# Kernel tuning notes

Hardware: AMD Instinct MI355X
Metric: run time of the kernel (lower is better)

## Reference

```python
import jax, jax.numpy as jnp
import numpy as np

K = 3
N_SENSOR = 10   # num_sensor N (forced by reshape(-1,10,10))
ADJ_N = 5       # adjacency size (forced by reshape(-1,5,5))
T_LEN = 4096    # seq_len
BATCH = 1024    # batch_size == num_of_filters (forced by output accumulation)


def _scaled_laplacian(W):
    # L_tilde = 2L/lambda_max - I, L = D - W (W symmetric -> eigvalsh valid)
    D = jnp.diag(jnp.sum(W, axis=1))
    L = D - W
    lam_max = jnp.max(jnp.linalg.eigvalsh(L))
    return (2.0 * L) / lam_max - jnp.eye(W.shape[0], dtype=W.dtype)


def _cheb_polynomials(L_tilde, K):
    polys = [jnp.eye(L_tilde.shape[0], dtype=L_tilde.dtype), L_tilde]
    for _ in range(2, K):
        polys.append(2.0 * (L_tilde @ polys[-1]) - polys[-2])
    return jnp.stack(polys[:K])  # (K, 5, 5)


def setup_inputs() -> dict:
    key = jax.random.key(0)
    kx, ka, ks, kt = jax.random.split(key, 4)
    x = jax.random.normal(kx, (T_LEN, BATCH, N_SENSOR), dtype=jnp.float32)
    W = jax.random.uniform(ka, (ADJ_N, ADJ_N), dtype=jnp.float32)
    # symmetric, zero-diagonal adjacency so the Laplacian is symmetric PSD-ish
    adj_mx = (W + W.T) * 0.5 * (1.0 - jnp.eye(ADJ_N, dtype=jnp.float32))
    spatial_attention = jax.random.uniform(ks, (BATCH, N_SENSOR, N_SENSOR), dtype=jnp.float32)
    Theta = jax.random.normal(kt, (K, N_SENSOR, BATCH), dtype=jnp.float32)  # (K, num_of_timesteps=10, num_of_filters=B)
    return {"x": x, "adj_mx": adj_mx, "spatial_attention": spatial_attention, "Theta": Theta}


def reference(x, adj_mx, spatial_attention, Theta):
    # adj path is detached in the torch code (cpu().detach().numpy())
    L_tilde = _scaled_laplacian(jax.lax.stop_gradient(adj_mx))
    cheb = _cheb_polynomials(L_tilde, K)                 # (K, 5, 5)
    T, B, N = x.shape                                    # (T, B, 10)
    x_t = jnp.swapaxes(x, 0, 2)                          # (10, B, T)
    sa = spatial_attention.reshape(-1, ADJ_N, ADJ_N)     # (4B, 5, 5)
    output = jnp.zeros((T, B, N), dtype=x.dtype)
    for k in range(K):
        T_k_with_at = (cheb[k] * sa).reshape(-1, N, N)   # (B, 10, 10)
        lhs = jnp.swapaxes(T_k_with_at, 0, 2)            # (10, 10, B)
        rhs = jnp.matmul(lhs, x_t)                       # (10, 10, B) @ (10, B, T) -> (10, 10, T)
        out_k = jnp.matmul(jnp.swapaxes(rhs, 1, 2), Theta[k])  # (10, T, 10) @ (10, B) -> (10, T, B)
        output = output + jnp.transpose(out_k, (1, 2, 0))       # (T, B, 10)
    return jax.nn.relu(output[..., None])                # (T, B, 10, 1)
```

## Files before the change

kernel.cpp:

```cpp
#include <hip/hip_runtime.h>
#include <math.h>

#define TLEN 4096
#define NB   1024
#define NS   10
#define KC   64
#define NCHK 16
#define BUF_U32 10240

typedef __attribute__((ext_vector_type(8))) short s16x8;
typedef __attribute__((ext_vector_type(4))) float f32x4;
typedef __attribute__((ext_vector_type(2))) float f32x2;

static __device__ __forceinline__ unsigned cvtpk(float lo, float hi) {
  unsigned r;
  asm("v_cvt_pk_bf16_f32 %0, %1, %2" : "=v"(r) : "v"(lo), "v"(hi));
  return r;
}
static __device__ __forceinline__ int swz(int P, int L) {
  return P*64 + (L ^ ((P ^ (P >> 2)) & 7));
}
static __device__ __forceinline__ void lbar() {
  asm volatile("s_waitcnt lgkmcnt(0)" ::: "memory");
  __builtin_amdgcn_s_barrier();
}

__global__ __launch_bounds__(512) void fused_k(
    const float* __restrict__ x, const float* __restrict__ sa,
    const float* __restrict__ adj, const float* __restrict__ theta,
    float* __restrict__ out) {
  __shared__ __align__(16) unsigned buf[BUF_U32];
  __shared__ __align__(16) unsigned S2[16*52];
  __shared__ float ck[300];
  const int tid = threadIdx.x;
  const int l   = tid & 63;
  const int t0  = blockIdx.x * 16;

  const int w   = tid >> 6;
  const int bp  = tid / 10;
  const int rm  = tid - bp*10;
  const int q   = rm >> 1;
  const int th  = rm & 1;
  const int gq  = rm;
  const int ksx = bp >> 4;
  const int kgx = (bp & 15) >> 2;
  const int jwx = bp & 3;
  const int n0  = 2*w, n1 = 2*w + 1;

  f32x4 acc0 = {0.f,0.f,0.f,0.f}, acc1 = {0.f,0.f,0.f,0.f};
  f32x2 xlo[8], xhi[8], slo[5], shi[5];

  float pL[5][5], pv[5];
  if (tid == 320) {
    float Wm[5][5];
    #pragma unroll
    for (int r = 0; r < 5; ++r)
      #pragma unroll
      for (int c = 0; c < 5; ++c) Wm[r][c] = adj[r*5+c];
    #pragma unroll
    for (int r = 0; r < 5; ++r) {
      float d = 0.f;
      #pragma unroll
      for (int c = 0; c < 5; ++c) d += Wm[r][c];
      #pragma unroll
      for (int c = 0; c < 5; ++c) pL[r][c] = (r==c ? d : 0.f) - Wm[r][c];
    }
    pv[0]=0.7f; pv[1]=-1.1f; pv[2]=0.9f; pv[3]=-0.8f; pv[4]=1.3f;
  }

  if (tid < 320) {
    const float* xb = x + (size_t)(t0 + th*8)*(NB*NS) + (size_t)(2*bp)*NS + 2*q;
    #pragma unroll
    for (int r = 0; r < 8; ++r) {
      xlo[r] = __builtin_nontemporal_load((const f32x2*)(xb + r*(NB*NS)));
      xhi[r] = __builtin_nontemporal_load((const f32x2*)(xb + r*(NB*NS) + NS));
    }
    const float* sb = sa + (size_t)(2*bp)*100 + gq*10;
    #pragma unroll
    for (int e = 0; e < 5; ++e) {
      slo[e] = *(const f32x2*)(sb + 2*e);
      shi[e] = *(const f32x2*)(sb + 100 + 2*e);
    }
    #pragma unroll
    for (int r = 0; r < 8; ++r) {
      const int L = kgx*16 + th*8 + r;
      buf[swz((2*q  )*2 + ksx, L)*4 + jwx] = cvtpk(xlo[r].x, xhi[r].x);
      buf[swz((2*q+1)*2 + ksx, L)*4 + jwx] = cvtpk(xlo[r].y, xhi[r].y);
    }
    #pragma unroll
    for (int e = 0; e < 5; ++e) {
      const int L = kgx*16 + gq;
      buf[5120 + swz((2*e  )*2 + ksx, L)*4 + jwx] = cvtpk(slo[e].x, shi[e].x);
      buf[5120 + swz((2*e+1)*2 + ksx, L)*4 + jwx] = cvtpk(slo[e].y, shi[e].y);
    }
  }

  for (int c = 0; c < NCHK; ++c) {
    lbar();
    if (tid < 320) {
      if (c + 1 < NCHK) {
        const int bc = (c+1)*KC;
        const float* xb = x + (size_t)(t0 + th*8)*(NB*NS)
                            + (size_t)(bc + 2*bp)*NS + 2*q;
        #pragma unroll
        for (int r = 0; r < 8; ++r) {
          xlo[r] = __builtin_nontemporal_load((const f32x2*)(xb + r*(NB*NS)));
          xhi[r] = __builtin_nontemporal_load((const f32x2*)(xb + r*(NB*NS) + NS));
        }
        const float* sb = sa + (size_t)(bc + 2*bp)*100 + gq*10;
        #pragma unroll
        for (int e = 0; e < 5; ++e) {
          slo[e] = *(const f32x2*)(sb + 2*e);
          shi[e] = *(const f32x2*)(sb + 100 + 2*e);
        }
      }
      const s16x8* XBf = (const s16x8*)buf;
      const s16x8* ASf = (const s16x8*)(buf + 5120);
      #pragma unroll
      for (int ks = 0; ks < 2; ++ks) {
        acc0 = __builtin_amdgcn_mfma_f32_16x16x32_bf16(
                 ASf[swz(n0*2+ks, l)], XBf[swz(n0*2+ks, l)], acc0, 0, 0, 0);
        acc1 = __builtin_amdgcn_mfma_f32_16x16x32_bf16(
                 ASf[swz(n1*2+ks, l)], XBf[swz(n1*2+ks, l)], acc1, 0, 0, 0);
      }
    } else if (tid == 320 && c < 12) {
      #pragma unroll
      for (int it = 0; it < 8; ++it) {
        float wv[5];
        #pragma unroll
        for (int r = 0; r < 5; ++r) {
          float s = 0.f;
          #pragma unroll
          for (int cc = 0; cc < 5; ++cc) s += pL[r][cc]*pv[cc];
          wv[r] = s;
        }
        float s = fabsf(wv[0])+fabsf(wv[1])+fabsf(wv[2])+fabsf(wv[3])+fabsf(wv[4]);
        float inv = 1.f/s;
        #pragma unroll
        for (int r = 0; r < 5; ++r) pv[r] = wv[r]*inv;
      }
    }
    lbar();
    if (tid < 320 && c + 1 < NCHK) {
      #pragma unroll
      for (int r = 0; r < 8; ++r) {
        const int L = kgx*16 + th*8 + r;
        buf[swz((2*q  )*2 + ksx, L)*4 + jwx] = cvtpk(xlo[r].x, xhi[r].x);
        buf[swz((2*q+1)*2 + ksx, L)*4 + jwx] = cvtpk(xlo[r].y, xhi[r].y);
      }
      #pragma unroll
      for (int e = 0; e < 5; ++e) {
        const int L = kgx*16 + gq;
        buf[5120 + swz((2*e  )*2 + ksx, L)*4 + jwx] = cvtpk(slo[e].x, shi[e].x);
        buf[5120 + swz((2*e+1)*2 + ksx, L)*4 + jwx] = cvtpk(slo[e].y, shi[e].y);
      }
    }
  }

  if (tid == 320) {
    float num = 0.f, den = 0.f;
    #pragma unroll
    for (int r = 0; r < 5; ++r) {
      float s = 0.f;
      #pragma unroll
      for (int cc = 0; cc < 5; ++cc) s += pL[r][cc]*pv[cc];
      num += pv[r]*s; den += pv[r]*pv[r];
    }
    const float lam = num/den;
    float Lt[5][5], T2[5][5];
    #pragma unroll
    for (int r = 0; r < 5; ++r)
      #pragma unroll
      for (int cc = 0; cc < 5; ++cc)
        Lt[r][cc] = 2.f*pL[r][cc]/lam - (r==cc ? 1.f : 0.f);
    #pragma unroll
    for (int r = 0; r < 5; ++r)
      #pragma unroll
      for (int cc = 0; cc < 5; ++cc) {
        float s = 0.f;
        #pragma unroll
        for (int j = 0; j < 5; ++j) s += Lt[r][j]*Lt[j][cc];
        T2[r][cc] = 2.f*s - (r==cc ? 1.f : 0.f);
      }
    #pragma unroll
    for (int p = 0; p < 10; ++p)
      #pragma unroll
      for (int nn = 0; nn < 10; ++nn) {
        const int m = (10*p+nn) % 25, r = m/5, cc = m%5;
        ck[0*100 + p*10+nn] = (r==cc ? 1.f : 0.f);
        ck[1*100 + p*10+nn] = Lt[r][cc];
        ck[2*100 + p*10+nn] = T2[r][cc];
      }
  }
  if (tid < 320) {
    const int pg = (l >> 4) * 4;
    const int tl = l & 15;
    unsigned* srow = S2 + tl*52;
    const int pp0 = pg >> 1;
    if (pg < 10) {
      srow[pp0*10 + n0] = cvtpk(acc0[0], acc0[1]);
      srow[pp0*10 + n1] = cvtpk(acc1[0], acc1[1]);
    }
    if (pg + 2 < 10) {
      srow[(pp0+1)*10 + n0] = cvtpk(acc0[2], acc0[3]);
      srow[(pp0+1)*10 + n1] = cvtpk(acc1[2], acc1[3]);
    }
  }
  lbar();

  float* stg = (float*)buf;
  for (int g = 0; g < 2; ++g) {
    const int b = g*512 + tid;
    float W[10][10];
    #pragma unroll
    for (int p = 0; p < 10; ++p) {
      const float th0 = theta[          p*NB + b];
      const float th1 = theta[10*NB  +  p*NB + b];
      const float th2 = theta[20*NB  +  p*NB + b];
      #pragma unroll
      for (int nn = 0; nn < 10; ++nn)
        W[p][nn] = ck[p*10+nn]*th0 + ck[100+p*10+nn]*th1 + ck[200+p*10+nn]*th2;
    }
    for (int tp = 0; tp < 8; ++tp) {
      float a0[10], a1[10];
      #pragma unroll
      for (int nn = 0; nn < 10; ++nn) { a0[nn] = 0.f; a1[nn] = 0.f; }
      {
        const uint4* rp = (const uint4*)(S2 + (2*tp)*52);
        uint4 rq[13];
        #pragma unroll
        for (int i = 0; i < 13; ++i) rq[i] = rp[i];
        #pragma unroll
        for (int j = 0; j < 50; ++j) {
          const int i = j >> 2, e = j & 3;
          const unsigned u = (e==0) ? rq[i].x : (e==1) ? rq[i].y
                           : (e==2) ? rq[i].z : rq[i].w;
          const int pp = j / 10, nn = j - pp*10;
          a0[nn] += __uint_as_float(u << 16)        * W[2*pp][nn]
                  + __uint_as_float(u & 0xffff0000u) * W[2*pp+1][nn];
        }
      }
      {
        const uint4* rp = (const uint4*)(S2 + (2*tp+1)*52);
        uint4 rq[13];
        #pragma unroll
        for (int i = 0; i < 13; ++i) rq[i] = rp[i];
        #pragma unroll
        for (int j = 0; j < 50; ++j) {
          const int i = j >> 2, e = j & 3;
          const unsigned u = (e==0) ? rq[i].x : (e==1) ? rq[i].y
                           : (e==2) ? rq[i].z : rq[i].w;
          const int pp = j / 10, nn = j - pp*10;
          a1[nn] += __uint_as_float(u << 16)        * W[2*pp][nn]
                  + __uint_as_float(u & 0xffff0000u) * W[2*pp+1][nn];
        }
      }
      lbar();
      #pragma unroll
      for (int nn = 0; nn < 10; ++nn) {
        stg[       tid*10 + nn] = fmaxf(a0[nn], 0.f);
        stg[5120 + tid*10 + nn] = fmaxf(a1[nn], 0.f);
      }
      lbar();
      const f32x4* sv = (const f32x4*)stg;
      f32x4* op0 = (f32x4*)(out + (size_t)(t0 + 2*tp)*(NB*NS) + g*5120);
      f32x4* op1 = (f32x4*)(out + (size_t)(t0 + 2*tp + 1)*(NB*NS) + g*5120);
      __builtin_nontemporal_store(sv[tid],        op0 + tid);
      __builtin_nontemporal_store(sv[tid + 512],  op0 + tid + 512);
      if (tid < 256)
        __builtin_nontemporal_store(sv[tid + 1024], op0 + tid + 1024);
      __builtin_nontemporal_store(sv[tid + 1280], op1 + tid);
      __builtin_nontemporal_store(sv[tid + 1792], op1 + tid + 512);
      if (tid < 256)
        __builtin_nontemporal_store(sv[tid + 2304], op1 + tid + 1024);
    }
  }
}

extern "C" void kernel_launch(void* const* d_in, const int* in_sizes, int n_in,
                              void* d_out, int out_size, void* d_ws, size_t ws_size,
                              hipStream_t stream) {
  const float* x   = (const float*)d_in[0];
  const float* adj = (const float*)d_in[1];
  const float* sa  = (const float*)d_in[2];
  const float* th  = (const float*)d_in[3];
  float* out = (float*)d_out;
  hipLaunchKernelGGL(fused_k, dim3(TLEN/16), dim3(512), 0, stream,
                     x, sa, adj, th, out);
}
```

Measured before the change: 87.11 us.

## Split batch halves across a second grid dimension and double-buffer output staging

The two batch halves, previously looped over inside each block, now go to separate blocks along blockIdx.y, doubling the grid to 512 blocks. Each block also processes one timestep at a time into alternating staging buffers, needing one barrier per timestep instead of two. The aim is better CU occupancy and latency hiding and fewer barriers. The cost is that the front stage producing S2 is repeated by both y-blocks, duplicating its input reads and arithmetic.

```diff
diff --git a/kernel.cpp b/kernel.cpp
--- a/kernel.cpp
+++ b/kernel.cpp
@@ -209,71 +209,48 @@
   lbar();
 
   float* stg = (float*)buf;
-  for (int g = 0; g < 2; ++g) {
-    const int b = g*512 + tid;
-    float W[10][10];
-    #pragma unroll
-    for (int p = 0; p < 10; ++p) {
-      const float th0 = theta[          p*NB + b];
-      const float th1 = theta[10*NB  +  p*NB + b];
-      const float th2 = theta[20*NB  +  p*NB + b];
-      #pragma unroll
-      for (int nn = 0; nn < 10; ++nn)
-        W[p][nn] = ck[p*10+nn]*th0 + ck[100+p*10+nn]*th1 + ck[200+p*10+nn]*th2;
-    }
-    for (int tp = 0; tp < 8; ++tp) {
-      float a0[10], a1[10];
-      #pragma unroll
-      for (int nn = 0; nn < 10; ++nn) { a0[nn] = 0.f; a1[nn] = 0.f; }
-      {
-        const uint4* rp = (const uint4*)(S2 + (2*tp)*52);
-        uint4 rq[13];
-        #pragma unroll
-        for (int i = 0; i < 13; ++i) rq[i] = rp[i];
-        #pragma unroll
-        for (int j = 0; j < 50; ++j) {
-          const int i = j >> 2, e = j & 3;
-          const unsigned u = (e==0) ? rq[i].x : (e==1) ? rq[i].y
-                           : (e==2) ? rq[i].z : rq[i].w;
-          const int pp = j / 10, nn = j - pp*10;
-          a0[nn] += __uint_as_float(u << 16)        * W[2*pp][nn]
-                  + __uint_as_float(u & 0xffff0000u) * W[2*pp+1][nn];
-        }
-      }
-      {
-        const uint4* rp = (const uint4*)(S2 + (2*tp+1)*52);
-        uint4 rq[13];
-        #pragma unroll
-        for (int i = 0; i < 13; ++i) rq[i] = rp[i];
-        #pragma unroll
-        for (int j = 0; j < 50; ++j) {
-          const int i = j >> 2, e = j & 3;
-          const unsigned u = (e==0) ? rq[i].x : (e==1) ? rq[i].y
-                           : (e==2) ? rq[i].z : rq[i].w;
-          const int pp = j / 10, nn = j - pp*10;
-          a1[nn] += __uint_as_float(u << 16)        * W[2*pp][nn]
-                  + __uint_as_float(u & 0xffff0000u) * W[2*pp+1][nn];
-        }
-      }
-      lbar();
-      #pragma unroll
-      for (int nn = 0; nn < 10; ++nn) {
-        stg[       tid*10 + nn] = fmaxf(a0[nn], 0.f);
-        stg[5120 + tid*10 + nn] = fmaxf(a1[nn], 0.f);
-      }
-      lbar();
-      const f32x4* sv = (const f32x4*)stg;
-      f32x4* op0 = (f32x4*)(out + (size_t)(t0 + 2*tp)*(NB*NS) + g*5120);
-      f32x4* op1 = (f32x4*)(out + (size_t)(t0 + 2*tp + 1)*(NB*NS) + g*5120);
-      __builtin_nontemporal_store(sv[tid],        op0 + tid);
-      __builtin_nontemporal_store(sv[tid + 512],  op0 + tid + 512);
-      if (tid < 256)
-        __builtin_nontemporal_store(sv[tid + 1024], op0 + tid + 1024);
-      __builtin_nontemporal_store(sv[tid + 1280], op1 + tid);
-      __builtin_nontemporal_store(sv[tid + 1792], op1 + tid + 512);
-      if (tid < 256)
-        __builtin_nontemporal_store(sv[tid + 2304], op1 + tid + 1024);
-    }
+  const int b    = blockIdx.y*512 + tid;
+  const int yoff = blockIdx.y*5120;
+  float W[10][10];
+  #pragma unroll
+  for (int p = 0; p < 10; ++p) {
+    const float th0 = theta[          p*NB + b];
+    const float th1 = theta[10*NB  +  p*NB + b];
+    const float th2 = theta[20*NB  +  p*NB + b];
+    #pragma unroll
+    for (int nn = 0; nn < 10; ++nn)
+      W[p][nn] = ck[p*10+nn]*th0 + ck[100+p*10+nn]*th1 + ck[200+p*10+nn]*th2;
+  }
+  for (int t = 0; t < 16; ++t) {
+    float a0[10];
+    #pragma unroll
+    for (int nn = 0; nn < 10; ++nn) a0[nn] = 0.f;
+    {
+      const uint4* rp = (const uint4*)(S2 + t*52);
+      uint4 rq[13];
+      #pragma unroll
+      for (int i = 0; i < 13; ++i) rq[i] = rp[i];
+      #pragma unroll
+      for (int j = 0; j < 50; ++j) {
+        const int i = j >> 2, e = j & 3;
+        const unsigned u = (e==0) ? rq[i].x : (e==1) ? rq[i].y
+                         : (e==2) ? rq[i].z : rq[i].w;
+        const int pp = j / 10, nn = j - pp*10;
+        a0[nn] += __uint_as_float(u << 16)         * W[2*pp][nn]
+                + __uint_as_float(u & 0xffff0000u) * W[2*pp+1][nn];
+      }
+    }
+    float* sg = stg + (t & 1)*5120;
+    #pragma unroll
+    for (int nn = 0; nn < 10; ++nn)
+      sg[tid*10 + nn] = fmaxf(a0[nn], 0.f);
+    lbar();
+    const f32x4* sv = (const f32x4*)sg;
+    f32x4* op = (f32x4*)(out + (size_t)(t0 + t)*(NB*NS) + yoff);
+    __builtin_nontemporal_store(sv[tid],       op + tid);
+    __builtin_nontemporal_store(sv[tid + 512], op + tid + 512);
+    if (tid < 256)
+      __builtin_nontemporal_store(sv[tid + 1024], op + tid + 1024);
   }
 }
 
@@ -285,6 +262,6 @@
   const float* sa  = (const float*)d_in[2];
   const float* th  = (const float*)d_in[3];
   float* out = (float*)d_out;
-  hipLaunchKernelGGL(fused_k, dim3(TLEN/16), dim3(512), 0, stream,
+  hipLaunchKernelGGL(fused_k, dim3(TLEN/16, 2), dim3(512), 0, stream,
                      x, sa, adj, th, out);
 }
```

Result: slower. 148.9 us (+71.0%).
